# Kernel optimization log

Measured on AMD Instinct MI355X. Metric: run time of the kernel, lower is better.

## Reference

```python
import jax, jax.numpy as jnp
import numpy as np

D = 1024   # d_model
E = 8      # num_experts
K = 2      # top-k routes per token
B = 8192   # tokens (== max_tokens)
CAP = 1280 # ceil(1.25 * 8192 / 8)


def setup_inputs() -> dict:
    key = jax.random.key(0)
    ks = jax.random.split(key, 11)
    s = 1.0 / np.sqrt(D)
    u = lambda k_, shp: jax.random.uniform(k_, shp, jnp.float32, -s, s)
    return {
        "x": jax.random.normal(ks[0], (B, D), jnp.float32),
        "W1": u(ks[1], (E, D, D)),
        "b1": u(ks[2], (E, D)),
        "W2": u(ks[3], (E, D, D)),
        "b2": u(ks[4], (E, D)),
        "Wf1": u(ks[5], (D, D)),
        "bf1": u(ks[6], (D,)),
        "Wf2": u(ks[7], (D, D)),
        "bf2": u(ks[8], (D,)),
        "routes": jax.random.randint(ks[9], (B, K), 0, E, jnp.int32),
        "capacity": CAP,
    }


def reference(x, W1, b1, W2, b2, Wf1, bf1, Wf2, bf2, routes, capacity):
    Bn, Dm = x.shape
    En = W1.shape[0]
    Kk = routes.shape[1]

    # --- capacity-aware acceptance (vectorized equivalent of the sequential loop) ---
    # A (token,slot) assignment to expert e is accepted iff the number of earlier
    # valid assignments to e (flattened token-major, slot-minor order) is < capacity.
    # This is exactly the torch loop semantics: load only grows on accept, and once
    # it hits capacity every later assignment to that expert is rejected.
    e = routes.reshape(-1)                                   # [B*K]
    valid = (e >= 0) & (e < En)
    e_safe = jnp.where(valid, e, 0)
    oh = jax.nn.one_hot(e_safe, En, dtype=jnp.int32) * valid[:, None].astype(jnp.int32)
    rank = jnp.cumsum(oh, axis=0) - oh                        # exclusive prefix count [B*K, E]
    rank_at = jnp.take_along_axis(rank, e_safe[:, None], axis=1)[:, 0]
    accept = (valid & (rank_at < capacity)).reshape(Bn, Kk)   # [B, K]

    # --- dense per-expert 2-layer MLP (grouped GEMM form) ---
    # torch Linear: y = x @ W.T + b, W is [out, in]
    h = jax.nn.relu(jnp.einsum('bd,ehd->ebh', x, W1) + b1[:, None, :])  # [E,B,D]
    y = jnp.einsum('ebh,eoh->ebo', h, W2) + b2[:, None, :]              # [E,B,D]

    # --- combine accepted expert outputs per token ---
    yt = jnp.transpose(y, (1, 0, 2))                          # [B,E,D]
    idx = e_safe.reshape(Bn, Kk)
    g = jnp.take_along_axis(yt, idx[:, :, None], axis=1)      # [B,K,D]
    af = accept.astype(x.dtype)
    summed = jnp.sum(af[:, :, None] * g, axis=1)              # [B,D]
    used = jnp.sum(af, axis=1)                                # [B]

    # --- fallback MLP for overflowed tokens ---
    fb = jax.nn.relu(x @ Wf1.T + bf1) @ Wf2.T + bf2

    out = jnp.where((used > 0)[:, None], summed / jnp.maximum(used, 1.0)[:, None], fb)
    return out
```

## Files before the change

### kernel.cpp

```cpp
#include <hip/hip_runtime.h>

#define DM    1024
#define NEXP  8
#define BTOK  8192
#define KTOP  2
#define NASSIGN (BTOK*KTOP)
#define CAPC  1280
#define MROWS (NEXP*CAPC)

#define NTILES   (DM/128)
#define SLOTS_E  (5*NTILES)
#define SLOTS_F  (32*NTILES/8)
#define SLOTS    (SLOTS_E+SLOTS_F)
#define GRID_L   (8*SLOTS)

typedef unsigned short ushort_t;
typedef __attribute__((ext_vector_type(8))) __bf16 bf16x8;
typedef __attribute__((ext_vector_type(4))) float  f32x4;

__device__ __forceinline__ ushort_t f2b(float f) {
  union { float f; unsigned u; } a; a.f = f;
  unsigned u = a.u;
  return (ushort_t)((u + 0x7FFFu + ((u >> 16) & 1u)) >> 16);
}
__device__ __forceinline__ float b2f(ushort_t h) {
  union { unsigned u; float f; } a; a.u = ((unsigned)h) << 16;
  return a.f;
}

#define GLOAD_LDS(g, l) __builtin_amdgcn_global_load_lds( \
    (const __attribute__((address_space(1))) void*)(g),   \
    (__attribute__((address_space(3))) void*)(l), 16, 0, 0)

__global__ void route_cvt_kernel(const int* __restrict__ routes, const int* __restrict__ capp,
                                 int* __restrict__ gidx, int* __restrict__ slot,
                                 int* __restrict__ counts, int* __restrict__ nfb,
                                 const float* __restrict__ W1, const float* __restrict__ W2,
                                 const float* __restrict__ Wf1, const float* __restrict__ Wf2,
                                 ushort_t* __restrict__ o1, ushort_t* __restrict__ o2,
                                 ushort_t* __restrict__ of1, ushort_t* __restrict__ of2) {
  const int b = blockIdx.x, t = threadIdx.x;
  if (b >= 8) {
    const float* s; ushort_t* d; int idx;
    int c = b - 8;
    if (c < 2048)      { s = W1;  d = o1;  idx = c; }
    else if (c < 4096) { s = W2;  d = o2;  idx = c - 2048; }
    else if (c < 4352) { s = Wf1; d = of1; idx = c - 4096; }
    else               { s = Wf2; d = of2; idx = c - 4352; }
    int i = idx * 1024 + t;
    float4 v = ((const float4*)s)[i];
    ushort4 o; o.x = f2b(v.x); o.y = f2b(v.y); o.z = f2b(v.z); o.w = f2b(v.w);
    ((ushort4*)d)[i] = o;
    return;
  }
  const int e = b;
  const int lane = t & 63, w = t >> 6;
  int cap = *capp; if (cap > CAPC) cap = CAPC;
  if (e == 0 && t == 0) *nfb = 0;
  __shared__ int wtot[16];
  int base = 0;
  for (int i0 = 0; i0 < NASSIGN; i0 += 1024) {
    int i = i0 + t;
    int r = routes[i];
    bool mine = (r == e);
    unsigned long long mask = __ballot(mine);
    int pre = __popcll(mask & ((1ull << lane) - 1ull));
    if (lane == 0) wtot[w] = __popcll(mask);
    __syncthreads();
    int tot = 0;
#pragma unroll
    for (int j = 0; j < 16; ++j) { int c = wtot[j]; if (j < w) pre += c; tot += c; }
    if (e == 0 && (unsigned)r >= NEXP) slot[i] = -1;
    if (mine) {
      int pos = base + pre;
      if (pos < cap) { gidx[e * CAPC + pos] = i >> 1; slot[i] = e * CAPC + pos; }
      else slot[i] = -1;
    }
    base += tot;
    __syncthreads();
  }
  if (t == 0) counts[e] = base < cap ? base : cap;
}

__global__ void fblist_gxg_kernel(const int* __restrict__ slot, int* __restrict__ fbidx,
                                  int* __restrict__ nfb,
                                  const float* __restrict__ x, const int* __restrict__ gidx,
                                  const int* __restrict__ counts, ushort_t* __restrict__ xg) {
  int b = blockIdx.x, t = threadIdx.x;
  if (b < 32) {
    int tok = b * 256 + t;
    int u = (slot[2 * tok] >= 0) + (slot[2 * tok + 1] >= 0);
    if (u == 0) { int p = atomicAdd(nfb, 1); fbidx[p] = tok; }
    return;
  }
  int row = b - 32;
  int e = row / CAPC, p = row % CAPC;
  int d = t * 4;
  ushort4 o = {0, 0, 0, 0};
  if (p < counts[e]) {
    int tok = gidx[row];
    float4 v = *(const float4*)(x + (size_t)tok * DM + d);
    o.x = f2b(v.x); o.y = f2b(v.y); o.z = f2b(v.z); o.w = f2b(v.w);
  }
  *(ushort4*)(xg + (size_t)row * DM + d) = o;
}

__global__ void gather_xf_kernel(const float* __restrict__ x, const int* __restrict__ fbidx,
                                 const int* __restrict__ nfbp, ushort_t* __restrict__ xf) {
  int row = blockIdx.x;
  int n = *nfbp;
  int nr = (n + 127) & ~127;
  if (row >= nr) return;
  int d = threadIdx.x * 4;
  ushort4 o = {0, 0, 0, 0};
  if (row < n) {
    int tok = fbidx[row];
    float4 v = *(const float4*)(x + (size_t)tok * DM + d);
    o.x = f2b(v.x); o.y = f2b(v.y); o.z = f2b(v.z); o.w = f2b(v.w);
  }
  *(ushort4*)(xf + (size_t)row * DM + d) = o;
}

template <int RELU, int FBSCAT>
__global__ __launch_bounds__(512, 4) void layer_kernel(
    const ushort_t* __restrict__ Ae, const ushort_t* __restrict__ We,
    const float* __restrict__ be, ushort_t* __restrict__ Ce,
    const ushort_t* __restrict__ Af, const ushort_t* __restrict__ Wf,
    const float* __restrict__ bfp, ushort_t* __restrict__ Cf,
    float* __restrict__ outF, const int* __restrict__ scat,
    const int* __restrict__ nfbp) {
  const int b = blockIdx.x;
  const int xcd = b & 7, s = b >> 3;
  const ushort_t* A; const ushort_t* W; const float* bias; ushort_t* C;
  int mgrp, ntile; bool isfb;
  if (s < SLOTS_E) {
    const int e = xcd;
    mgrp = e * 5 + (s >> 3); ntile = s & 7;
    A = Ae; W = We + (size_t)e * DM * DM; bias = be + e * DM; C = Ce; isfb = false;
  } else {
    int fl = (s - SLOTS_E) * 8 + xcd;
    mgrp = fl >> 3; ntile = fl & 7;
    if (mgrp * 256 >= *nfbp) return;
    A = Af; W = Wf; bias = bfp; C = Cf; isfb = true;
  }
  const int tid = threadIdx.x, lane = tid & 63, w = tid >> 6;
  const int wr = w >> 1, wc = w & 1;
  __shared__ ushort_t smem[24576];
  const size_t Abase = (size_t)mgrp * 256 * DM;
  const size_t Wbase = (size_t)ntile * 128 * DM;
  f32x4 acc[4][4] = {};

  const int sub  = lane >> 2;
  const int slt  = lane & 3;
  const int gcol = (slt ^ ((sub >> 1) & 3)) * 8;
  const int ra0 = (w * 2)     * 16 + sub;
  const int ra1 = (w * 2 + 1) * 16 + sub;
  const int rbw = w * 16 + sub;

#define STAGE(T, BUF) do { int kt_ = (T) * 32;                                        \
    GLOAD_LDS(A + Abase + (size_t)ra0 * DM + kt_ + gcol, smem + (BUF)*8192 + (w*2)  *512); \
    GLOAD_LDS(A + Abase + (size_t)ra1 * DM + kt_ + gcol, smem + (BUF)*8192 + (w*2+1)*512); \
    GLOAD_LDS(W + Wbase + (size_t)rbw * DM + kt_ + gcol, smem + 16384 + (BUF)*4096 + w*512); \
  } while (0)

  const int fr    = lane & 15, g = lane >> 4;
  const int rslot = (g ^ ((fr >> 1) & 3)) * 8;

  STAGE(0, 0);
  for (int t = 0; t < 32; ++t) {
    __syncthreads();
    if (t + 1 < 32) STAGE(t + 1, (t + 1) & 1);
    const ushort_t* bA = smem + (t & 1) * 8192;
    const ushort_t* bB = smem + 16384 + (t & 1) * 4096;
    bf16x8 av[4], bv[4];
#pragma unroll
    for (int m = 0; m < 4; ++m)
      av[m] = *(const bf16x8*)&bA[(wr * 64 + m * 16 + fr) * 32 + rslot];
#pragma unroll
    for (int n = 0; n < 4; ++n)
      bv[n] = *(const bf16x8*)&bB[(wc * 64 + n * 16 + fr) * 32 + rslot];
#pragma unroll
    for (int m = 0; m < 4; ++m)
#pragma unroll
      for (int n = 0; n < 4; ++n)
        acc[m][n] = __builtin_amdgcn_mfma_f32_16x16x32_bf16(av[m], bv[n], acc[m][n], 0, 0, 0);
  }
#undef STAGE

  if (FBSCAT && isfb) {
    int nfbv = *nfbp;
#pragma unroll
    for (int n = 0; n < 4; ++n) {
      int col = ntile * 128 + wc * 64 + n * 16 + fr;
      float bb = bias[col];
#pragma unroll
      for (int m = 0; m < 4; ++m) {
        int row0 = mgrp * 256 + wr * 64 + m * 16 + g * 4;
#pragma unroll
        for (int r = 0; r < 4; ++r) {
          int row = row0 + r;
          if (row < nfbv) outF[(size_t)scat[row] * DM + col] = acc[m][n][r] + bb;
        }
      }
    }
  } else {
    ushort_t* Cb = C + (size_t)mgrp * 256 * DM + ntile * 128;
#pragma unroll
    for (int h = 0; h < 2; ++h) {
      __syncthreads();
      if ((wr >> 1) == h) {
#pragma unroll
        for (int n = 0; n < 4; ++n) {
          int col = wc * 64 + n * 16 + fr;
          float bb = bias[ntile * 128 + col];
#pragma unroll
          for (int m = 0; m < 4; ++m) {
            int lrow0 = (wr & 1) * 64 + m * 16 + g * 4;
#pragma unroll
            for (int r = 0; r < 4; ++r) {
              float v = acc[m][n][r] + bb;
              if (RELU) v = v > 0.0f ? v : 0.0f;
              smem[(lrow0 + r) * 128 + col] = f2b(v);
            }
          }
        }
      }
      __syncthreads();
#pragma unroll
      for (int q = 0; q < 4; ++q) {
        int chunk = q * 512 + tid;
        int row = chunk >> 4, co = (chunk & 15) * 8;
        bf16x8 v = *(const bf16x8*)&smem[row * 128 + co];
        *(bf16x8*)(Cb + (size_t)(h * 128 + row) * DM + co) = v;
      }
    }
  }
}

__global__ void combine_kernel(const ushort_t* __restrict__ Y, const int* __restrict__ slot,
                               float* __restrict__ out) {
  int t = blockIdx.x;
  int s0 = slot[2 * t], s1 = slot[2 * t + 1];
  int u = (s0 >= 0) + (s1 >= 0);
  if (u == 0) return;
  int d = threadIdx.x * 4;
  float a0 = 0, a1 = 0, a2 = 0, a3 = 0;
  if (s0 >= 0) {
    ushort4 q = *(const ushort4*)(Y + (size_t)s0 * DM + d);
    a0 += b2f(q.x); a1 += b2f(q.y); a2 += b2f(q.z); a3 += b2f(q.w);
  }
  if (s1 >= 0) {
    ushort4 q = *(const ushort4*)(Y + (size_t)s1 * DM + d);
    a0 += b2f(q.x); a1 += b2f(q.y); a2 += b2f(q.z); a3 += b2f(q.w);
  }
  float inv = 1.0f / (float)u;
  float4 o = make_float4(a0 * inv, a1 * inv, a2 * inv, a3 * inv);
  *(float4*)(out + (size_t)t * DM + d) = o;
}

extern "C" void kernel_launch(void* const* d_in, const int* in_sizes, int n_in,
                              void* d_out, int out_size, void* d_ws, size_t ws_size,
                              hipStream_t stream) {
  const float* x   = (const float*)d_in[0];
  const float* W1  = (const float*)d_in[1];
  const float* b1  = (const float*)d_in[2];
  const float* W2  = (const float*)d_in[3];
  const float* b2  = (const float*)d_in[4];
  const float* Wf1 = (const float*)d_in[5];
  const float* bf1 = (const float*)d_in[6];
  const float* Wf2 = (const float*)d_in[7];
  const float* bf2 = (const float*)d_in[8];
  const int* routes = (const int*)d_in[9];
  const int* capp   = (const int*)d_in[10];
  float* out = (float*)d_out;

  char* ws = (char*)d_ws;
  size_t off = 0;
  auto alloc = [&](size_t bytes) -> void* {
    void* p = ws + off; off += (bytes + 255) & ~255ull; return p;
  };
  ushort_t* W1b  = (ushort_t*)alloc((size_t)NEXP * DM * DM * 2);
  ushort_t* W2b  = (ushort_t*)alloc((size_t)NEXP * DM * DM * 2);
  ushort_t* Wf1b = (ushort_t*)alloc((size_t)DM * DM * 2);
  ushort_t* Wf2b = (ushort_t*)alloc((size_t)DM * DM * 2);
  ushort_t* xg   = (ushort_t*)alloc((size_t)MROWS * DM * 2);
  ushort_t* H    = (ushort_t*)alloc((size_t)MROWS * DM * 2);
  ushort_t* Y    = (ushort_t*)alloc((size_t)MROWS * DM * 2);
  ushort_t* xf   = (ushort_t*)alloc((size_t)BTOK * DM * 2);
  ushort_t* Hf   = (ushort_t*)alloc((size_t)BTOK * DM * 2);
  int* gidx   = (int*)alloc(MROWS * 4);
  int* slot   = (int*)alloc(NASSIGN * 4);
  int* counts = (int*)alloc(NEXP * 4);
  int* fbidx  = (int*)alloc(BTOK * 4);
  int* nfb    = (int*)alloc(4);

  route_cvt_kernel<<<8 + 4608, 1024, 0, stream>>>(routes, capp, gidx, slot, counts, nfb,
                                                  W1, W2, Wf1, Wf2, W1b, W2b, Wf1b, Wf2b);
  fblist_gxg_kernel<<<32 + MROWS, 256, 0, stream>>>(slot, fbidx, nfb, x, gidx, counts, xg);
  gather_xf_kernel<<<BTOK, 256, 0, stream>>>(x, fbidx, nfb, xf);
  layer_kernel<1, 0><<<GRID_L, 512, 0, stream>>>(xg, W1b, b1, H, xf, Wf1b, bf1, Hf,
                                                 nullptr, nullptr, nfb);
  layer_kernel<0, 1><<<GRID_L, 512, 0, stream>>>(H, W2b, b2, Y, Hf, Wf2b, bf2, nullptr,
                                                 out, fbidx, nfb);
  combine_kernel<<<BTOK, 256, 0, stream>>>(Y, slot, out);
}
```

Before: 128.5 us.

## Fuse token gather into GEMM A-loads and scatter-add expert outputs into output

Converts x to bf16 once inside the prep kernel. The first layer then loads A rows indirectly through gidx/fbidx, using a zero row for padding, so the separate gather kernels and gathered copies of x go away. The second layer's expert path atomically adds bias-added outputs, scaled by a precomputed 1/used, straight into a zeroed output, which removes the Y buffer and the combine kernel. The cost is a memset of the output, float atomics in the epilogue with nondeterministic summation order, and indirect row addressing in the GEMM loads.

```diff
diff --git a/kernel.cpp b/kernel.cpp
--- a/kernel.cpp
+++ b/kernel.cpp
@@ -23,10 +23,6 @@
   unsigned u = a.u;
   return (ushort_t)((u + 0x7FFFu + ((u >> 16) & 1u)) >> 16);
 }
-__device__ __forceinline__ float b2f(ushort_t h) {
-  union { unsigned u; float f; } a; a.u = ((unsigned)h) << 16;
-  return a.f;
-}
 
 #define GLOAD_LDS(g, l) __builtin_amdgcn_global_load_lds( \
     (const __attribute__((address_space(1))) void*)(g),   \
@@ -34,29 +30,37 @@
 
 __global__ void route_cvt_kernel(const int* __restrict__ routes, const int* __restrict__ capp,
                                  int* __restrict__ gidx, int* __restrict__ slot,
-                                 int* __restrict__ counts, int* __restrict__ nfb,
+                                 int* __restrict__ nfb, int* __restrict__ fbidx,
                                  const float* __restrict__ W1, const float* __restrict__ W2,
                                  const float* __restrict__ Wf1, const float* __restrict__ Wf2,
                                  ushort_t* __restrict__ o1, ushort_t* __restrict__ o2,
-                                 ushort_t* __restrict__ of1, ushort_t* __restrict__ of2) {
+                                 ushort_t* __restrict__ of1, ushort_t* __restrict__ of2,
+                                 const float* __restrict__ x, ushort_t* __restrict__ xb) {
   const int b = blockIdx.x, t = threadIdx.x;
   if (b >= 8) {
-    const float* s; ushort_t* d; int idx;
     int c = b - 8;
-    if (c < 2048)      { s = W1;  d = o1;  idx = c; }
-    else if (c < 4096) { s = W2;  d = o2;  idx = c - 2048; }
-    else if (c < 4352) { s = Wf1; d = of1; idx = c - 4096; }
-    else               { s = Wf2; d = of2; idx = c - 4352; }
-    int i = idx * 1024 + t;
-    float4 v = ((const float4*)s)[i];
-    ushort4 o; o.x = f2b(v.x); o.y = f2b(v.y); o.z = f2b(v.z); o.w = f2b(v.w);
-    ((ushort4*)d)[i] = o;
+    if (c < 6656) {
+      const float* s; ushort_t* d; int idx;
+      if (c < 2048)      { s = W1;  d = o1;  idx = c; }
+      else if (c < 4096) { s = W2;  d = o2;  idx = c - 2048; }
+      else if (c < 4352) { s = Wf1; d = of1; idx = c - 4096; }
+      else if (c < 4608) { s = Wf2; d = of2; idx = c - 4352; }
+      else               { s = x;   d = xb;  idx = c - 4608; }
+      int i = idx * 1024 + t;
+      float4 v = ((const float4*)s)[i];
+      ushort4 o; o.x = f2b(v.x); o.y = f2b(v.y); o.z = f2b(v.z); o.w = f2b(v.w);
+      ((ushort4*)d)[i] = o;
+    } else if (t < 256) {
+      ushort4 z = {0, 0, 0, 0};
+      ((ushort4*)(xb + (size_t)BTOK * DM))[t] = z;
+    }
     return;
   }
   const int e = b;
   const int lane = t & 63, w = t >> 6;
   int cap = *capp; if (cap > CAPC) cap = CAPC;
   if (e == 0 && t == 0) *nfb = 0;
+  fbidx[e * 1024 + t] = BTOK;
   __shared__ int wtot[16];
   int base = 0;
   for (int i0 = 0; i0 < NASSIGN; i0 += 1024) {
@@ -79,55 +83,28 @@
     base += tot;
     __syncthreads();
   }
-  if (t == 0) counts[e] = base < cap ? base : cap;
-}
-
-__global__ void fblist_gxg_kernel(const int* __restrict__ slot, int* __restrict__ fbidx,
-                                  int* __restrict__ nfb,
-                                  const float* __restrict__ x, const int* __restrict__ gidx,
-                                  const int* __restrict__ counts, ushort_t* __restrict__ xg) {
-  int b = blockIdx.x, t = threadIdx.x;
-  if (b < 32) {
-    int tok = b * 256 + t;
-    int u = (slot[2 * tok] >= 0) + (slot[2 * tok + 1] >= 0);
-    if (u == 0) { int p = atomicAdd(nfb, 1); fbidx[p] = tok; }
-    return;
-  }
-  int row = b - 32;
-  int e = row / CAPC, p = row % CAPC;
-  int d = t * 4;
-  ushort4 o = {0, 0, 0, 0};
-  if (p < counts[e]) {
-    int tok = gidx[row];
-    float4 v = *(const float4*)(x + (size_t)tok * DM + d);
-    o.x = f2b(v.x); o.y = f2b(v.y); o.z = f2b(v.z); o.w = f2b(v.w);
-  }
-  *(ushort4*)(xg + (size_t)row * DM + d) = o;
-}
-
-__global__ void gather_xf_kernel(const float* __restrict__ x, const int* __restrict__ fbidx,
-                                 const int* __restrict__ nfbp, ushort_t* __restrict__ xf) {
-  int row = blockIdx.x;
-  int n = *nfbp;
-  int nr = (n + 127) & ~127;
-  if (row >= nr) return;
-  int d = threadIdx.x * 4;
-  ushort4 o = {0, 0, 0, 0};
-  if (row < n) {
-    int tok = fbidx[row];
-    float4 v = *(const float4*)(x + (size_t)tok * DM + d);
-    o.x = f2b(v.x); o.y = f2b(v.y); o.z = f2b(v.z); o.w = f2b(v.w);
-  }
-  *(ushort4*)(xf + (size_t)row * DM + d) = o;
-}
-
-template <int RELU, int FBSCAT>
+  int cnt = base < cap ? base : cap;
+  for (int pos = cnt + t; pos < CAPC; pos += 1024)
+    gidx[e * CAPC + pos] = BTOK;
+}
+
+__global__ void fblist_kernel(const int* __restrict__ slot, int* __restrict__ fbidx,
+                              int* __restrict__ nfb, float* __restrict__ invu) {
+  int tok = blockIdx.x * 256 + threadIdx.x;
+  if (tok >= BTOK) return;
+  int u = (slot[2 * tok] >= 0) + (slot[2 * tok + 1] >= 0);
+  invu[tok] = u ? 1.0f / (float)u : 0.0f;
+  if (u == 0) { int p = atomicAdd(nfb, 1); fbidx[p] = tok; }
+}
+
+template <int LAYER>
 __global__ __launch_bounds__(512, 4) void layer_kernel(
     const ushort_t* __restrict__ Ae, const ushort_t* __restrict__ We,
     const float* __restrict__ be, ushort_t* __restrict__ Ce,
     const ushort_t* __restrict__ Af, const ushort_t* __restrict__ Wf,
     const float* __restrict__ bfp, ushort_t* __restrict__ Cf,
-    float* __restrict__ outF, const int* __restrict__ scat,
+    float* __restrict__ outF, const int* __restrict__ gidxp,
+    const int* __restrict__ fbidxp, const float* __restrict__ invu,
     const int* __restrict__ nfbp) {
   const int b = blockIdx.x;
   const int xcd = b & 7, s = b >> 3;
@@ -146,7 +123,6 @@
   const int tid = threadIdx.x, lane = tid & 63, w = tid >> 6;
   const int wr = w >> 1, wc = w & 1;
   __shared__ ushort_t smem[24576];
-  const size_t Abase = (size_t)mgrp * 256 * DM;
   const size_t Wbase = (size_t)ntile * 128 * DM;
   f32x4 acc[4][4] = {};
 
@@ -157,9 +133,20 @@
   const int ra1 = (w * 2 + 1) * 16 + sub;
   const int rbw = w * 16 + sub;
 
+  size_t sA0, sA1;
+  if (LAYER == 1) {
+    int row0 = mgrp * 256 + ra0, row1 = mgrp * 256 + ra1;
+    int t0 = isfb ? fbidxp[row0] : gidxp[row0];
+    int t1 = isfb ? fbidxp[row1] : gidxp[row1];
+    sA0 = (size_t)t0 * DM; sA1 = (size_t)t1 * DM;
+  } else {
+    sA0 = (size_t)(mgrp * 256 + ra0) * DM;
+    sA1 = (size_t)(mgrp * 256 + ra1) * DM;
+  }
+
 #define STAGE(T, BUF) do { int kt_ = (T) * 32;                                        \
-    GLOAD_LDS(A + Abase + (size_t)ra0 * DM + kt_ + gcol, smem + (BUF)*8192 + (w*2)  *512); \
-    GLOAD_LDS(A + Abase + (size_t)ra1 * DM + kt_ + gcol, smem + (BUF)*8192 + (w*2+1)*512); \
+    GLOAD_LDS(A + sA0 + kt_ + gcol, smem + (BUF)*8192 + (w*2)  *512);                 \
+    GLOAD_LDS(A + sA1 + kt_ + gcol, smem + (BUF)*8192 + (w*2+1)*512);                 \
     GLOAD_LDS(W + Wbase + (size_t)rbw * DM + kt_ + gcol, smem + 16384 + (BUF)*4096 + w*512); \
   } while (0)
 
@@ -187,19 +174,37 @@
   }
 #undef STAGE
 
-  if (FBSCAT && isfb) {
-    int nfbv = *nfbp;
-#pragma unroll
-    for (int n = 0; n < 4; ++n) {
-      int col = ntile * 128 + wc * 64 + n * 16 + fr;
-      float bb = bias[col];
-#pragma unroll
-      for (int m = 0; m < 4; ++m) {
-        int row0 = mgrp * 256 + wr * 64 + m * 16 + g * 4;
-#pragma unroll
-        for (int r = 0; r < 4; ++r) {
-          int row = row0 + r;
-          if (row < nfbv) outF[(size_t)scat[row] * DM + col] = acc[m][n][r] + bb;
+  if (LAYER == 2) {
+    if (isfb) {
+      int nfbv = *nfbp;
+#pragma unroll
+      for (int n = 0; n < 4; ++n) {
+        int col = ntile * 128 + wc * 64 + n * 16 + fr;
+        float bb = bias[col];
+#pragma unroll
+        for (int m = 0; m < 4; ++m) {
+          int row0 = mgrp * 256 + wr * 64 + m * 16 + g * 4;
+#pragma unroll
+          for (int r = 0; r < 4; ++r) {
+            int row = row0 + r;
+            if (row < nfbv) outF[(size_t)fbidxp[row] * DM + col] = acc[m][n][r] + bb;
+          }
+        }
+      }
+    } else {
+#pragma unroll
+      for (int n = 0; n < 4; ++n) {
+        int col = ntile * 128 + wc * 64 + n * 16 + fr;
+        float bb = bias[col];
+#pragma unroll
+        for (int m = 0; m < 4; ++m) {
+          int row0 = mgrp * 256 + wr * 64 + m * 16 + g * 4;
+#pragma unroll
+          for (int r = 0; r < 4; ++r) {
+            int tok = gidxp[row0 + r];
+            if (tok != BTOK)
+              atomicAdd(outF + (size_t)tok * DM + col, (acc[m][n][r] + bb) * invu[tok]);
+          }
         }
       }
     }
@@ -219,7 +224,7 @@
 #pragma unroll
             for (int r = 0; r < 4; ++r) {
               float v = acc[m][n][r] + bb;
-              if (RELU) v = v > 0.0f ? v : 0.0f;
+              v = v > 0.0f ? v : 0.0f;
               smem[(lrow0 + r) * 128 + col] = f2b(v);
             }
           }
@@ -235,27 +240,6 @@
       }
     }
   }
-}
-
-__global__ void combine_kernel(const ushort_t* __restrict__ Y, const int* __restrict__ slot,
-                               float* __restrict__ out) {
-  int t = blockIdx.x;
-  int s0 = slot[2 * t], s1 = slot[2 * t + 1];
-  int u = (s0 >= 0) + (s1 >= 0);
-  if (u == 0) return;
-  int d = threadIdx.x * 4;
-  float a0 = 0, a1 = 0, a2 = 0, a3 = 0;
-  if (s0 >= 0) {
-    ushort4 q = *(const ushort4*)(Y + (size_t)s0 * DM + d);
-    a0 += b2f(q.x); a1 += b2f(q.y); a2 += b2f(q.z); a3 += b2f(q.w);
-  }
-  if (s1 >= 0) {
-    ushort4 q = *(const ushort4*)(Y + (size_t)s1 * DM + d);
-    a0 += b2f(q.x); a1 += b2f(q.y); a2 += b2f(q.z); a3 += b2f(q.w);
-  }
-  float inv = 1.0f / (float)u;
-  float4 o = make_float4(a0 * inv, a1 * inv, a2 * inv, a3 * inv);
-  *(float4*)(out + (size_t)t * DM + d) = o;
 }
 
 extern "C" void kernel_launch(void* const* d_in, const int* in_sizes, int n_in,
@@ -283,24 +267,22 @@
   ushort_t* W2b  = (ushort_t*)alloc((size_t)NEXP * DM * DM * 2);
   ushort_t* Wf1b = (ushort_t*)alloc((size_t)DM * DM * 2);
   ushort_t* Wf2b = (ushort_t*)alloc((size_t)DM * DM * 2);
-  ushort_t* xg   = (ushort_t*)alloc((size_t)MROWS * DM * 2);
+  ushort_t* xb   = (ushort_t*)alloc((size_t)(BTOK + 1) * DM * 2);
   ushort_t* H    = (ushort_t*)alloc((size_t)MROWS * DM * 2);
-  ushort_t* Y    = (ushort_t*)alloc((size_t)MROWS * DM * 2);
-  ushort_t* xf   = (ushort_t*)alloc((size_t)BTOK * DM * 2);
   ushort_t* Hf   = (ushort_t*)alloc((size_t)BTOK * DM * 2);
-  int* gidx   = (int*)alloc(MROWS * 4);
-  int* slot   = (int*)alloc(NASSIGN * 4);
-  int* counts = (int*)alloc(NEXP * 4);
-  int* fbidx  = (int*)alloc(BTOK * 4);
-  int* nfb    = (int*)alloc(4);
-
-  route_cvt_kernel<<<8 + 4608, 1024, 0, stream>>>(routes, capp, gidx, slot, counts, nfb,
-                                                  W1, W2, Wf1, Wf2, W1b, W2b, Wf1b, Wf2b);
-  fblist_gxg_kernel<<<32 + MROWS, 256, 0, stream>>>(slot, fbidx, nfb, x, gidx, counts, xg);
-  gather_xf_kernel<<<BTOK, 256, 0, stream>>>(x, fbidx, nfb, xf);
-  layer_kernel<1, 0><<<GRID_L, 512, 0, stream>>>(xg, W1b, b1, H, xf, Wf1b, bf1, Hf,
-                                                 nullptr, nullptr, nfb);
-  layer_kernel<0, 1><<<GRID_L, 512, 0, stream>>>(H, W2b, b2, Y, Hf, Wf2b, bf2, nullptr,
-                                                 out, fbidx, nfb);
-  combine_kernel<<<BTOK, 256, 0, stream>>>(Y, slot, out);
-}
+  int*   gidx  = (int*)alloc(MROWS * 4);
+  int*   slot  = (int*)alloc(NASSIGN * 4);
+  int*   fbidx = (int*)alloc(BTOK * 4);
+  float* invu  = (float*)alloc(BTOK * 4);
+  int*   nfb   = (int*)alloc(4);
+
+  hipMemsetAsync(out, 0, (size_t)out_size * 4, stream);
+  route_cvt_kernel<<<6665, 1024, 0, stream>>>(routes, capp, gidx, slot, nfb, fbidx,
+                                              W1, W2, Wf1, Wf2, W1b, W2b, Wf1b, Wf2b,
+                                              x, xb);
+  fblist_kernel<<<BTOK / 256, 256, 0, stream>>>(slot, fbidx, nfb, invu);
+  layer_kernel<1><<<GRID_L, 512, 0, stream>>>(xb, W1b, b1, H, xb, Wf1b, bf1, Hf,
+                                              nullptr, gidx, fbidx, invu, nfb);
+  layer_kernel<2><<<GRID_L, 512, 0, stream>>>(H, W2b, b2, nullptr, Hf, Wf2b, bf2, nullptr,
+                                              out, gidx, fbidx, invu, nfb);
+}
```

Result: slower. 139.1 us (+8.3%).
